# Kernel optimization log

Hardware: AMD Instinct MI355X
Metric: run time of the kernel (lower is better)

The kernel has to match this reference:

```python
import jax, jax.numpy as jnp
import numpy as np

BETA = 1.0
THRESHOLD = 20.0
TOP_K = 2
NUM_EXPERTS = 64


def softplus(x):
    # matches torch module: clamp arg at threshold, passthrough above
    x_beta = BETA * x
    soft = (1.0 / BETA) * jnp.log1p(jnp.exp(jnp.minimum(x_beta, THRESHOLD)))
    return jnp.where(x_beta > THRESHOLD, x, soft)


def setup_inputs() -> dict:
    key = jax.random.key(0)
    k1, k2, k3, k4 = jax.random.split(key, 4)
    B, S, D, E = 4, 4096, 2048, NUM_EXPERTS
    std = (2.0 / (D + E)) ** 0.5
    x = jax.random.normal(k1, (B, S, D), dtype=jnp.float32)
    W_topk = jax.random.truncated_normal(k2, -3.0, 3.0, (E, D), dtype=jnp.float32) * std
    W_noise = jax.random.truncated_normal(k3, -3.0, 3.0, (E, D), dtype=jnp.float32) * std
    noise = jax.random.normal(k4, (B, S, E), dtype=jnp.float32)
    return {"x": x, "W_topk": W_topk, "W_noise": W_noise, "noise": noise}


def reference(x, W_topk, W_noise, noise):
    # two small projections: [B,S,D] x [E,D] -> [B,S,E]
    raw_logits = jnp.einsum('bsd,ed->bse', x, W_topk)
    raw_noise_logits = jnp.einsum('bsd,ed->bse', x, W_noise)
    combined = softplus(raw_noise_logits) * noise + raw_logits

    top_k_values, top_k_indices = jax.lax.top_k(combined, TOP_K)  # [B,S,K]

    # scatter top-k values into a -inf tensor along the expert dim
    expert_ids = jnp.arange(NUM_EXPERTS)
    onehot = top_k_indices[..., :, None] == expert_ids  # [B,S,K,E] bool
    scattered = jnp.sum(jnp.where(onehot, top_k_values[..., :, None], 0.0), axis=-2)  # [B,S,E]
    selected = jnp.any(onehot, axis=-2)  # [B,S,E]
    new_logits = jnp.where(selected, scattered, -jnp.inf)

    probs = jax.nn.softmax(new_logits, axis=-1)
    return probs, top_k_indices
```

## Files before the change

### kernel.cpp

```cpp
#include <hip/hip_runtime.h>
#include <math.h>

#define NTOK 16384
#define DDIM 2048
#define NEXP 64
#define TOKB 32
#define KQ   512
#define KC   64
#define NCHUNK 8
#define ROWB 144
#define PLANEB 4608
#define REGS 9232
#define HPLANE 262144
#define SCALE 4096.0f
#define UNSCALE (1.0f / (SCALE * SCALE))

typedef _Float16 half8 __attribute__((ext_vector_type(8)));
typedef float    f32x4 __attribute__((ext_vector_type(4)));

__global__ __launch_bounds__(256) void pack_w(const float* __restrict__ Wt,
                                              const float* __restrict__ Wn,
                                              _Float16* __restrict__ WB) {
    int t  = blockIdx.x * 256 + threadIdx.x;
    int e  = t >> 8;
    int k8 = t & 255;
    int k  = k8 * 8;
    const float* src = ((e < NEXP) ? (Wt + (size_t)e * DDIM)
                                   : (Wn + (size_t)(e - NEXP) * DDIM)) + k;
    int n = e >> 4, ei = e & 15, ks = k8 >> 2, q = k8 & 3;
    size_t off = (((size_t)n * 64 + ks) * 64 + (q * 16 + ei)) * 8;
    half8 h0, h1;
#pragma unroll
    for (int j = 0; j < 8; ++j) {
        float v = src[j] * SCALE;
        _Float16 a = (_Float16)v;
        h0[j] = a;
        h1[j] = (_Float16)(v - (float)a);
    }
    *(half8*)(WB + off)          = h0;
    *(half8*)(WB + HPLANE + off) = h1;
}

__global__ __launch_bounds__(512, 4) void router_main(const float* __restrict__ x,
                                                      const _Float16* __restrict__ WB,
                                                      const float* __restrict__ noise,
                                                      float* __restrict__ out) {
    __shared__ float smem[4 * 128 * 33];
    char* stg = (char*)smem;

    const int tid  = threadIdx.x;
    const int lane = tid & 63;
    const int w    = tid >> 6;
    const int eh   = w & 1;
    const int kh   = w >> 1;
    const int tok0 = blockIdx.x * TOKB;

    f32x4 acc[2][4];
#pragma unroll
    for (int tt = 0; tt < 2; ++tt)
#pragma unroll
        for (int t = 0; t < 4; ++t) acc[tt][t] = (f32x4){0.f, 0.f, 0.f, 0.f};

    const int stok = tid >> 4;
    const int seg  = tid & 15;
    const int khs  = seg >> 2;
    const int kk   = (seg & 3) * 16;
    const float* xrow = x + (size_t)(tok0 + stok) * DDIM + khs * KQ + kk;
    char* wlo = stg + khs * REGS + stok * ROWB + kk * 2;

    float4 xr[4];

#define LOADX(c)                                                        \
    {                                                                   \
        const float* p = xrow + (c) * KC;                               \
        xr[0] = *(const float4*)(p);                                    \
        xr[1] = *(const float4*)(p + 4);                                \
        xr[2] = *(const float4*)(p + 8);                                \
        xr[3] = *(const float4*)(p + 12);                               \
    }

#define STAGE()                                                         \
    {                                                                   \
        float v[16] = {xr[0].x, xr[0].y, xr[0].z, xr[0].w,              \
                       xr[1].x, xr[1].y, xr[1].z, xr[1].w,              \
                       xr[2].x, xr[2].y, xr[2].z, xr[2].w,              \
                       xr[3].x, xr[3].y, xr[3].z, xr[3].w};             \
        half8 L0, L1, H0, H1;                                           \
        _Pragma("unroll")                                               \
        for (int m = 0; m < 8; ++m) {                                   \
            float s0 = v[m] * SCALE;                                    \
            float s1 = v[8 + m] * SCALE;                                \
            _Float16 a0 = (_Float16)s0, a1 = (_Float16)s1;              \
            L0[m] = a0;  L1[m] = a1;                                    \
            H0[m] = (_Float16)(s0 - (float)a0);                         \
            H1[m] = (_Float16)(s1 - (float)a1);                         \
        }                                                               \
        *(half8*)(wlo)               = L0;                              \
        *(half8*)(wlo + 16)          = L1;                              \
        *(half8*)(wlo + PLANEB)      = H0;                              \
        *(half8*)(wlo + PLANEB + 16) = H1;                              \
    }

    const char* abase = stg + kh * REGS + (lane & 15) * ROWB + ((lane >> 4) * 16);
    const _Float16* bb = WB + (((size_t)(eh * 4) * 64 + (size_t)kh * 16) * 64 + lane) * 8;

    LOADX(0);
    STAGE();
    __syncthreads();

    for (int c = 0; c < NCHUNK; ++c) {
        if (c + 1 < NCHUNK) LOADX(c + 1);
        const _Float16* bc = bb + (size_t)c * 1024;
#pragma unroll
        for (int ks = 0; ks < 2; ++ks) {
            half8 aL0 = *(const half8*)(abase + ks * 64);
            half8 aH0 = *(const half8*)(abase + ks * 64 + PLANEB);
            half8 aL1 = *(const half8*)(abase + 16 * ROWB + ks * 64);
            half8 aH1 = *(const half8*)(abase + 16 * ROWB + ks * 64 + PLANEB);
#pragma unroll
            for (int t = 0; t < 4; ++t) {
                const _Float16* bp = bc + ks * 512 + (size_t)t * 32768;
                half8 b0 = *(const half8*)(bp);
                half8 b1 = *(const half8*)(bp + HPLANE);
                acc[0][t] = __builtin_amdgcn_mfma_f32_16x16x32_f16(aL0, b0, acc[0][t], 0, 0, 0);
                acc[0][t] = __builtin_amdgcn_mfma_f32_16x16x32_f16(aH0, b0, acc[0][t], 0, 0, 0);
                acc[0][t] = __builtin_amdgcn_mfma_f32_16x16x32_f16(aL0, b1, acc[0][t], 0, 0, 0);
                acc[1][t] = __builtin_amdgcn_mfma_f32_16x16x32_f16(aL1, b0, acc[1][t], 0, 0, 0);
                acc[1][t] = __builtin_amdgcn_mfma_f32_16x16x32_f16(aH1, b0, acc[1][t], 0, 0, 0);
                acc[1][t] = __builtin_amdgcn_mfma_f32_16x16x32_f16(aL1, b1, acc[1][t], 0, 0, 0);
            }
        }
        __syncthreads();
        if (c + 1 < NCHUNK) {
            STAGE();
            __syncthreads();
        }
    }

    float* pw = smem;
#pragma unroll
    for (int tt = 0; tt < 2; ++tt)
#pragma unroll
        for (int t = 0; t < 4; ++t) {
            int e    = eh * 64 + t * 16 + (lane & 15);
            int tokl = tt * 16 + ((lane >> 4) << 2);
            int base = (kh * 128 + e) * 33 + tokl;
#pragma unroll
            for (int r = 0; r < 4; ++r)
                pw[base + r] = acc[tt][t][r] * UNSCALE;
        }
    __syncthreads();

    {
        int e  = tid >> 2;
        int t0 = (tid & 3) * 8;
#pragma unroll
        for (int j = 0; j < 8; ++j) {
            int tk = t0 + j;
            float s = pw[(0 * 128 + e) * 33 + tk] + pw[(1 * 128 + e) * 33 + tk]
                    + pw[(2 * 128 + e) * 33 + tk] + pw[(3 * 128 + e) * 33 + tk];
            pw[e * 33 + tk] = s;
        }
    }
    __syncthreads();

    float4* pt  = (float4*)(smem + 4224);
    float4* fin = (float4*)(smem + 4224 + 2048);

    {
        const int ptok = tid & 31;
        const int eg   = tid >> 5;
        float v1 = -INFINITY, v2 = -INFINITY;
        int i1 = 0, i2 = 0;
        float4 nz = *(const float4*)(noise + (size_t)(tok0 + ptok) * NEXP + eg * 4);
        float nzv[4] = {nz.x, nz.y, nz.z, nz.w};
#pragma unroll
        for (int cc = 0; cc < 4; ++cc) {
            int e = eg * 4 + cc;
            float lg = pw[e * 33 + ptok];
            float nl = pw[(NEXP + e) * 33 + ptok];
            float soft = log1pf(expf(fminf(nl, 20.f)));
            float cmb  = ((nl > 20.f) ? nl : soft) * nzv[cc] + lg;
            if (cmb > v1)      { v2 = v1; i2 = i1; v1 = cmb; i1 = e; }
            else if (cmb > v2) { v2 = cmb; i2 = e; }
        }
        pt[eg * 32 + ptok] = make_float4(v1, (float)i1, v2, (float)i2);
    }
    __syncthreads();

    if (tid < 32) {
        float4 g = pt[tid];
        float v1 = g.x, v2 = g.z;
        int i1 = (int)g.y, i2 = (int)g.w;
#pragma unroll
        for (int gg = 1; gg < 16; ++gg) {
            float4 p = pt[gg * 32 + tid];
            if (p.x > v1)      { v2 = v1; i2 = i1; v1 = p.x; i1 = (int)p.y; }
            else if (p.x > v2) { v2 = p.x; i2 = (int)p.y; }
            if (p.z > v1)      { v2 = v1; i2 = i1; v1 = p.z; i1 = (int)p.w; }
            else if (p.z > v2) { v2 = p.z; i2 = (int)p.w; }
        }
        float e2  = expf(v2 - v1);
        float inv = 1.f / (1.f + e2);
        fin[tid] = make_float4((float)i1, (float)i2, inv, e2 * inv);
    }
    __syncthreads();

    {
        const int tok = tid >> 4;
        const int sg  = tid & 15;
        float4 f = fin[tok];
        int i1 = (int)f.x, i2 = (int)f.y;
        float o[4];
#pragma unroll
        for (int cc = 0; cc < 4; ++cc) {
            int e = sg * 4 + cc;
            o[cc] = (e == i1) ? f.z : ((e == i2) ? f.w : 0.f);
        }
        *(float4*)(out + (size_t)(tok0 + tok) * NEXP + sg * 4) =
            make_float4(o[0], o[1], o[2], o[3]);
    }
    if (tid < 32) {
        float4 f = fin[tid];
        *(float2*)(out + (size_t)NTOK * NEXP + (size_t)(tok0 + tid) * 2) = make_float2(f.x, f.y);
    }
#undef LOADX
#undef STAGE
}

extern "C" void kernel_launch(void* const* d_in, const int* in_sizes, int n_in,
                              void* d_out, int out_size, void* d_ws, size_t ws_size,
                              hipStream_t stream) {
    const float* x  = (const float*)d_in[0];
    const float* Wt = (const float*)d_in[1];
    const float* Wn = (const float*)d_in[2];
    const float* nz = (const float*)d_in[3];
    float* out = (float*)d_out;
    _Float16* WB = (_Float16*)d_ws;

    hipLaunchKernelGGL(pack_w, dim3(128), dim3(256), 0, stream, Wt, Wn, WB);
    hipLaunchKernelGGL(router_main, dim3(NTOK / TOKB), dim3(512), 0, stream, x, WB, nz, out);
}
```

Before: 216.4 us.

## Load x fragments directly from global into MFMA registers, dropping LDS staging

```diff
diff --git a/kernel.cpp b/kernel.cpp
--- a/kernel.cpp
+++ b/kernel.cpp
@@ -5,12 +5,6 @@
 #define DDIM 2048
 #define NEXP 64
 #define TOKB 32
-#define KQ   512
-#define KC   64
-#define NCHUNK 8
-#define ROWB 144
-#define PLANEB 4608
-#define REGS 9232
 #define HPLANE 262144
 #define SCALE 4096.0f
 #define UNSCALE (1.0f / (SCALE * SCALE))
@@ -41,12 +35,24 @@
     *(half8*)(WB + HPLANE + off) = h1;
 }
 
+#define CVT(lo4, hi4, L, H)                                             \
+    {                                                                   \
+        float vv[8] = {lo4.x, lo4.y, lo4.z, lo4.w,                      \
+                       hi4.x, hi4.y, hi4.z, hi4.w};                     \
+        _Pragma("unroll")                                               \
+        for (int m = 0; m < 8; ++m) {                                   \
+            float s = vv[m] * SCALE;                                    \
+            _Float16 a = (_Float16)s;                                   \
+            L[m] = a;                                                   \
+            H[m] = (_Float16)(s - (float)a);                            \
+        }                                                               \
+    }
+
 __global__ __launch_bounds__(512, 4) void router_main(const float* __restrict__ x,
                                                       const _Float16* __restrict__ WB,
                                                       const float* __restrict__ noise,
                                                       float* __restrict__ out) {
-    __shared__ float smem[4 * 128 * 33];
-    char* stg = (char*)smem;
+    __shared__ float pw[4 * 128 * 33];
 
     const int tid  = threadIdx.x;
     const int lane = tid & 63;
@@ -61,83 +67,35 @@
 #pragma unroll
         for (int t = 0; t < 4; ++t) acc[tt][t] = (f32x4){0.f, 0.f, 0.f, 0.f};
 
-    const int stok = tid >> 4;
-    const int seg  = tid & 15;
-    const int khs  = seg >> 2;
-    const int kk   = (seg & 3) * 16;
-    const float* xrow = x + (size_t)(tok0 + stok) * DDIM + khs * KQ + kk;
-    char* wlo = stg + khs * REGS + stok * ROWB + kk * 2;
-
-    float4 xr[4];
-
-#define LOADX(c)                                                        \
-    {                                                                   \
-        const float* p = xrow + (c) * KC;                               \
-        xr[0] = *(const float4*)(p);                                    \
-        xr[1] = *(const float4*)(p + 4);                                \
-        xr[2] = *(const float4*)(p + 8);                                \
-        xr[3] = *(const float4*)(p + 12);                               \
-    }
-
-#define STAGE()                                                         \
-    {                                                                   \
-        float v[16] = {xr[0].x, xr[0].y, xr[0].z, xr[0].w,              \
-                       xr[1].x, xr[1].y, xr[1].z, xr[1].w,              \
-                       xr[2].x, xr[2].y, xr[2].z, xr[2].w,              \
-                       xr[3].x, xr[3].y, xr[3].z, xr[3].w};             \
-        half8 L0, L1, H0, H1;                                           \
-        _Pragma("unroll")                                               \
-        for (int m = 0; m < 8; ++m) {                                   \
-            float s0 = v[m] * SCALE;                                    \
-            float s1 = v[8 + m] * SCALE;                                \
-            _Float16 a0 = (_Float16)s0, a1 = (_Float16)s1;              \
-            L0[m] = a0;  L1[m] = a1;                                    \
-            H0[m] = (_Float16)(s0 - (float)a0);                         \
-            H1[m] = (_Float16)(s1 - (float)a1);                         \
-        }                                                               \
-        *(half8*)(wlo)               = L0;                              \
-        *(half8*)(wlo + 16)          = L1;                              \
-        *(half8*)(wlo + PLANEB)      = H0;                              \
-        *(half8*)(wlo + PLANEB + 16) = H1;                              \
-    }
-
-    const char* abase = stg + kh * REGS + (lane & 15) * ROWB + ((lane >> 4) * 16);
+    const float* a0 = x + (size_t)(tok0 + (lane & 15)) * DDIM + kh * 512 + ((lane >> 4) * 8);
+    const float* a1 = a0 + (size_t)16 * DDIM;
     const _Float16* bb = WB + (((size_t)(eh * 4) * 64 + (size_t)kh * 16) * 64 + lane) * 8;
 
-    LOADX(0);
-    STAGE();
-    __syncthreads();
-
-    for (int c = 0; c < NCHUNK; ++c) {
-        if (c + 1 < NCHUNK) LOADX(c + 1);
-        const _Float16* bc = bb + (size_t)c * 1024;
 #pragma unroll
-        for (int ks = 0; ks < 2; ++ks) {
-            half8 aL0 = *(const half8*)(abase + ks * 64);
-            half8 aH0 = *(const half8*)(abase + ks * 64 + PLANEB);
-            half8 aL1 = *(const half8*)(abase + 16 * ROWB + ks * 64);
-            half8 aH1 = *(const half8*)(abase + 16 * ROWB + ks * 64 + PLANEB);
+    for (int ks = 0; ks < 16; ++ks) {
+        const float* ap0 = a0 + ks * 32;
+        const float* ap1 = a1 + ks * 32;
+        float4 xl0 = *(const float4*)(ap0);
+        float4 xh0 = *(const float4*)(ap0 + 4);
+        float4 xl1 = *(const float4*)(ap1);
+        float4 xh1 = *(const float4*)(ap1 + 4);
+        half8 aL0, aH0, aL1, aH1;
+        CVT(xl0, xh0, aL0, aH0);
+        CVT(xl1, xh1, aL1, aH1);
+        const _Float16* bp = bb + (size_t)ks * 512;
 #pragma unroll
-            for (int t = 0; t < 4; ++t) {
-                const _Float16* bp = bc + ks * 512 + (size_t)t * 32768;
-                half8 b0 = *(const half8*)(bp);
-                half8 b1 = *(const half8*)(bp + HPLANE);
-                acc[0][t] = __builtin_amdgcn_mfma_f32_16x16x32_f16(aL0, b0, acc[0][t], 0, 0, 0);
-                acc[0][t] = __builtin_amdgcn_mfma_f32_16x16x32_f16(aH0, b0, acc[0][t], 0, 0, 0);
-                acc[0][t] = __builtin_amdgcn_mfma_f32_16x16x32_f16(aL0, b1, acc[0][t], 0, 0, 0);
-                acc[1][t] = __builtin_amdgcn_mfma_f32_16x16x32_f16(aL1, b0, acc[1][t], 0, 0, 0);
-                acc[1][t] = __builtin_amdgcn_mfma_f32_16x16x32_f16(aH1, b0, acc[1][t], 0, 0, 0);
-                acc[1][t] = __builtin_amdgcn_mfma_f32_16x16x32_f16(aL1, b1, acc[1][t], 0, 0, 0);
-            }
-        }
-        __syncthreads();
-        if (c + 1 < NCHUNK) {
-            STAGE();
-            __syncthreads();
+        for (int t = 0; t < 4; ++t) {
+            half8 b0 = *(const half8*)(bp + (size_t)t * 32768);
+            half8 b1 = *(const half8*)(bp + (size_t)t * 32768 + HPLANE);
+            acc[0][t] = __builtin_amdgcn_mfma_f32_16x16x32_f16(aL0, b0, acc[0][t], 0, 0, 0);
+            acc[0][t] = __builtin_amdgcn_mfma_f32_16x16x32_f16(aH0, b0, acc[0][t], 0, 0, 0);
+            acc[0][t] = __builtin_amdgcn_mfma_f32_16x16x32_f16(aL0, b1, acc[0][t], 0, 0, 0);
+            acc[1][t] = __builtin_amdgcn_mfma_f32_16x16x32_f16(aL1, b0, acc[1][t], 0, 0, 0);
+            acc[1][t] = __builtin_amdgcn_mfma_f32_16x16x32_f16(aH1, b0, acc[1][t], 0, 0, 0);
+            acc[1][t] = __builtin_amdgcn_mfma_f32_16x16x32_f16(aL1, b1, acc[1][t], 0, 0, 0);
         }
     }
 
-    float* pw = smem;
 #pragma unroll
     for (int tt = 0; tt < 2; ++tt)
 #pragma unroll
@@ -164,8 +122,8 @@
     }
     __syncthreads();
 
-    float4* pt  = (float4*)(smem + 4224);
-    float4* fin = (float4*)(smem + 4224 + 2048);
+    float4* pt  = (float4*)(pw + 4224);
+    float4* fin = (float4*)(pw + 4224 + 2048);
 
     {
         const int ptok = tid & 31;
@@ -224,8 +182,6 @@
         float4 f = fin[tid];
         *(float2*)(out + (size_t)NTOK * NEXP + (size_t)(tok0 + tid) * 2) = make_float2(f.x, f.y);
     }
-#undef LOADX
-#undef STAGE
 }
 
 extern "C" void kernel_launch(void* const* d_in, const int* in_sizes, int n_in,
```

New measurement: 234.7 us. 1.08x slower.
